# Kernel tuning notes

Hardware: AMD Instinct MI355X
Metric: run time of the kernel (lower is better)

## Reference

```python
import jax, jax.numpy as jnp
import numpy as np

D1, D2, DK, NH = 1024, 1024, 1024, 1
B, S = 4, 2048


def setup_inputs() -> dict:
    key = jax.random.key(0)
    ks = jax.random.split(key, 12)
    scale1 = 1.0 / np.sqrt(D1)
    scale2 = 1.0 / np.sqrt(D2)
    scalek = 1.0 / np.sqrt(DK)
    return {
        "x": jax.random.normal(ks[0], (B, S, D1), dtype=jnp.float32),
        "y": jax.random.normal(ks[1], (B, S, D2), dtype=jnp.float32),
        "adj": jax.random.uniform(ks[2], (B, S, S), dtype=jnp.float32),
        "Wq": jax.random.uniform(ks[3], (D1, DK), jnp.float32, -scale1, scale1),
        "bq": jax.random.uniform(ks[4], (DK,), jnp.float32, -scale1, scale1),
        "Wk": jax.random.uniform(ks[5], (D2, DK), jnp.float32, -scale2, scale2),
        "bk": jax.random.uniform(ks[6], (DK,), jnp.float32, -scale2, scale2),
        "Wv": jax.random.uniform(ks[7], (D2, DK), jnp.float32, -scale2, scale2),
        "bv": jax.random.uniform(ks[8], (DK,), jnp.float32, -scale2, scale2),
        "Wo": jax.random.uniform(ks[9], (DK, D2), jnp.float32, -scalek, scalek),
        "bo": jax.random.uniform(ks[10], (D2,), jnp.float32, -scalek, scalek),
    }


def reference(x, y, adj, Wq, bq, Wk, bk, Wv, bv, Wo, bo):
    # Single-head (n_heads=1) cross-attention with additive adjacency bias.
    dk_head = DK // NH
    norm = 1.0 / np.sqrt(DK)
    Q = (x @ Wq + bq).reshape(NH, B, S, dk_head)   # [h,b,s,d]
    K = (y @ Wk + bk).reshape(NH, B, S, dk_head)
    V = (y @ Wv + bv).reshape(NH, B, S, dk_head)
    att = jnp.einsum('hbsd,hbtd->hbst', Q, K) * norm  # [h,b,s,t]
    att = jax.nn.softmax(att + adj, axis=-1)          # adj [b,s,t] broadcasts over h
    tmp = jnp.einsum('hbst,hbtd->hbsd', att, V).reshape(B, S, -1)  # [b,s,dk]
    out = (tmp @ Wo + bo).reshape(-1, S, D2)
    return out
```

## Files before the change

### kernel.cpp

```cpp
#include <hip/hip_runtime.h>
#include <stdint.h>

typedef unsigned short u16;
using bf16x8 = __attribute__((ext_vector_type(8))) short;
using f32x4  = __attribute__((ext_vector_type(4))) float;

#define NORM 0.03125f

enum { M_PROJ = 0, M_EXP = 1, M_PV = 2, M_OUT = 3 };

__device__ __forceinline__ u16 f2bf(float f) {
  uint32_t u = __float_as_uint(f);
  return (u16)((u + 0x7FFFu + ((u >> 16) & 1u)) >> 16);
}

__device__ __forceinline__ void gload_lds16(const void* g, void* lds) {
  __builtin_amdgcn_global_load_lds(
      (const __attribute__((address_space(1))) uint32_t*)g,
      (__attribute__((address_space(3))) uint32_t*)lds, 16, 0, 0);
}

__global__ void k_cvt(const float* __restrict__ in, u16* __restrict__ out, int n4) {
  int i = blockIdx.x * blockDim.x + threadIdx.x;
  if (i >= n4) return;
  float4 v = ((const float4*)in)[i];
  uint32_t lo = f2bf(v.x) | ((uint32_t)f2bf(v.y) << 16);
  uint32_t hi = f2bf(v.z) | ((uint32_t)f2bf(v.w) << 16);
  ((uint2*)out)[i] = make_uint2(lo, hi);
}

__global__ void k_tc(const float* __restrict__ W0, const float* __restrict__ W1,
                     const float* __restrict__ W2, const float* __restrict__ W3,
                     u16* __restrict__ dst) {
  __shared__ float t[64][65];
  const float* W = blockIdx.z == 0 ? W0 : blockIdx.z == 1 ? W1 : blockIdx.z == 2 ? W2 : W3;
  u16* WT = dst + (size_t)blockIdx.z * (1024 * 1024);
  int c0 = blockIdx.x * 64, r0 = blockIdx.y * 64;
  int c = threadIdx.x & 63, q = threadIdx.x >> 6;
  for (int r = q; r < 64; r += 4) t[r][c] = W[(size_t)(r0 + r) * 1024 + c0 + c];
  __syncthreads();
  for (int r = q; r < 64; r += 4) WT[(size_t)(c0 + r) * 1024 + r0 + c] = f2bf(t[c][r]);
}

struct GArgs {
  const u16* A; const u16* B; int lda, ldb; long long bstrideB; int K;
  const float* bias; const float* adj; float* dpart; const float* dpart_r;
  void* C; int ldc;
  const u16* A1; const u16* B1; const u16* B2;
  const float* bias1; const float* bias2; void* C1; void* C2;
};

template <int MODE>
__global__ __launch_bounds__(256, 4) void gemm_occ(GArgs g) {
  __shared__ __align__(16) u16 As[128 * 64];
  __shared__ __align__(16) u16 Bs[128 * 64];

  const int tid = threadIdx.x;
  const int lane = tid & 63;
  const int wid = tid >> 6;
  const int wr = wid >> 1, wc = wid & 1;

  const int m0 = blockIdx.x * 128;
  const int n0 = blockIdx.y * 128;
  const int b = m0 >> 11;

  const u16* A = g.A; const u16* B = g.B;
  const float* bias = g.bias; void* C = g.C;
  int zmode = 0;
  if constexpr (MODE == M_PROJ) {
    int z = blockIdx.z; zmode = z;
    if (z == 1) { A = g.A1; B = g.B1; bias = g.bias1; C = g.C1; }
    else if (z == 2) { A = g.A1; B = g.B2; bias = g.bias2; C = g.C2; }
  }
  const int lda = g.lda, ldb = g.ldb, K = g.K;
  const u16* Bp = B + (size_t)b * g.bstrideB;

  f32x4 acc[4][4] = {};

  const int ric = lane >> 3;
  const int c8 = (lane & 7) * 8;

  const int fr = lane & 15;
  const int hi = lane >> 4;

  for (int kt = 0; kt < K; kt += 64) {
#pragma unroll
    for (int c = 0; c < 4; ++c) {
      int ch = wid * 4 + c;
      int row = ch * 8 + ric;
      int swc = c8 ^ ((row & 7) << 3);
      gload_lds16(A + (size_t)(m0 + row) * lda + kt + swc, (void*)&As[ch * 512]);
      gload_lds16(Bp + (size_t)(n0 + row) * ldb + kt + swc, (void*)&Bs[ch * 512]);
    }
    __syncthreads();
#pragma unroll
    for (int kk = 0; kk < 64; kk += 32) {
      bf16x8 af[4], bfr[4];
#pragma unroll
      for (int m = 0; m < 4; ++m) {
        int row = wr * 64 + m * 16 + fr;
        af[m] = *(const bf16x8*)__builtin_assume_aligned(
            &As[row * 64 + ((kk + hi * 8) ^ ((row & 7) << 3))], 16);
      }
#pragma unroll
      for (int n = 0; n < 4; ++n) {
        int row = wc * 64 + n * 16 + fr;
        bfr[n] = *(const bf16x8*)__builtin_assume_aligned(
            &Bs[row * 64 + ((kk + hi * 8) ^ ((row & 7) << 3))], 16);
      }
#pragma unroll
      for (int m = 0; m < 4; ++m)
#pragma unroll
        for (int n = 0; n < 4; ++n)
          acc[m][n] = __builtin_amdgcn_mfma_f32_16x16x32_bf16(af[m], bfr[n], acc[m][n], 0, 0, 0);
    }
    __syncthreads();
  }

  const int lr = lane >> 4;
  const int lc = lane & 15;

  if constexpr (MODE == M_PROJ) {
    if (zmode < 2) {
      u16* Cc = (u16*)C;
#pragma unroll
      for (int m = 0; m < 4; ++m)
#pragma unroll
        for (int n = 0; n < 4; ++n) {
          int gcol = n0 + wc * 64 + n * 16 + lc;
          float bv = bias[gcol];
#pragma unroll
          for (int r = 0; r < 4; ++r) {
            int grow = m0 + wr * 64 + m * 16 + lr * 4 + r;
            Cc[(size_t)grow * g.ldc + gcol] = f2bf(acc[m][n][r] + bv);
          }
        }
    } else {
      u16* Cc = (u16*)C;
#pragma unroll
      for (int m = 0; m < 4; ++m) {
        int grow0 = m0 + wr * 64 + m * 16 + lr * 4;
        int t0 = grow0 & 2047;
#pragma unroll
        for (int n = 0; n < 4; ++n) {
          int gcol = n0 + wc * 64 + n * 16 + lc;
          float bv = bias[gcol];
          ushort4 pk = make_ushort4(f2bf(acc[m][n][0] + bv), f2bf(acc[m][n][1] + bv),
                                    f2bf(acc[m][n][2] + bv), f2bf(acc[m][n][3] + bv));
          *(ushort4*)&Cc[((size_t)b * 1024 + gcol) * 2048 + t0] = pk;
        }
      }
    }
  } else if constexpr (MODE == M_EXP) {
    u16* Cc = (u16*)C;
    float esum[4][4] = {};
#pragma unroll
    for (int m = 0; m < 4; ++m)
#pragma unroll
      for (int n = 0; n < 4; ++n) {
        int gcol = n0 + wc * 64 + n * 16 + lc;
#pragma unroll
        for (int r = 0; r < 4; ++r) {
          int grow = m0 + wr * 64 + m * 16 + lr * 4 + r;
          float z = acc[m][n][r] * NORM + g.adj[(size_t)grow * 2048 + gcol];
          float e = __expf(z);
          Cc[(size_t)grow * 2048 + gcol] = f2bf(e);
          esum[m][r] += e;
        }
      }
    int pidx = blockIdx.y * 2 + wc;
#pragma unroll
    for (int m = 0; m < 4; ++m)
#pragma unroll
      for (int r = 0; r < 4; ++r) {
        float s = esum[m][r];
        s += __shfl_xor(s, 1); s += __shfl_xor(s, 2);
        s += __shfl_xor(s, 4); s += __shfl_xor(s, 8);
        if (lc == 0)
          g.dpart[(size_t)pidx * 8192 + (m0 + wr * 64 + m * 16 + lr * 4 + r)] = s;
      }
  } else if constexpr (MODE == M_PV) {
    __shared__ float dinv[128];
    if (tid < 128) {
      float s = 0.f;
#pragma unroll
      for (int t = 0; t < 32; ++t) s += g.dpart_r[(size_t)t * 8192 + m0 + tid];
      dinv[tid] = 1.0f / s;
    }
    __syncthreads();
    u16* Cc = (u16*)C;
#pragma unroll
    for (int m = 0; m < 4; ++m)
#pragma unroll
      for (int n = 0; n < 4; ++n) {
        int gcol = n0 + wc * 64 + n * 16 + lc;
#pragma unroll
        for (int r = 0; r < 4; ++r) {
          int lrow = wr * 64 + m * 16 + lr * 4 + r;
          Cc[(size_t)(m0 + lrow) * g.ldc + gcol] = f2bf(acc[m][n][r] * dinv[lrow]);
        }
      }
  } else {
    float* Cc = (float*)C;
#pragma unroll
    for (int m = 0; m < 4; ++m)
#pragma unroll
      for (int n = 0; n < 4; ++n) {
        int gcol = n0 + wc * 64 + n * 16 + lc;
        float bv = bias[gcol];
#pragma unroll
        for (int r = 0; r < 4; ++r) {
          int grow = m0 + wr * 64 + m * 16 + lr * 4 + r;
          Cc[(size_t)grow * g.ldc + gcol] = acc[m][n][r] + bv;
        }
      }
  }
}

extern "C" void kernel_launch(void* const* d_in, const int* in_sizes, int n_in,
                              void* d_out, int out_size, void* d_ws, size_t ws_size,
                              hipStream_t stream) {
  const float* x   = (const float*)d_in[0];
  const float* y   = (const float*)d_in[1];
  const float* adj = (const float*)d_in[2];
  const float* Wq  = (const float*)d_in[3];
  const float* bq  = (const float*)d_in[4];
  const float* Wk  = (const float*)d_in[5];
  const float* bk  = (const float*)d_in[6];
  const float* Wv  = (const float*)d_in[7];
  const float* bv  = (const float*)d_in[8];
  const float* Wo  = (const float*)d_in[9];
  const float* bo  = (const float*)d_in[10];
  float* out = (float*)d_out;

  char* ws = (char*)d_ws;
  if (ws_size < 143654912ULL) return;
  u16* xb = (u16*)(ws);
  u16* yb = (u16*)(ws + 16777216);
  u16* WT = (u16*)(ws + 33554432);
  u16* Qb = (u16*)(ws + 41943040);
  u16* Kb = (u16*)(ws + 58720256);
  u16* Vt = (u16*)(ws + 75497472);
  u16* E  = (u16*)(ws + 92274688);
  float* dpart = (float*)(ws + 125829120);
  u16* tmpb = (u16*)(ws + 126877696);

  u16* WqT = WT;
  u16* WkT = WT + 1048576;
  u16* WvT = WT + 2097152;
  u16* WoT = WT + 3145728;

  k_cvt<<<8192, 256, 0, stream>>>(x, xb, 2097152);
  k_cvt<<<8192, 256, 0, stream>>>(y, yb, 2097152);
  k_tc<<<dim3(16, 16, 4), 256, 0, stream>>>(Wq, Wk, Wv, Wo, WT);

  GArgs ga;
  ga.A = xb; ga.B = WqT; ga.lda = 1024; ga.ldb = 1024; ga.bstrideB = 0; ga.K = 1024;
  ga.bias = bq; ga.adj = nullptr; ga.dpart = nullptr; ga.dpart_r = nullptr;
  ga.C = Qb; ga.ldc = 1024;
  ga.A1 = yb; ga.B1 = WkT; ga.B2 = WvT; ga.bias1 = bk; ga.bias2 = bv;
  ga.C1 = Kb; ga.C2 = Vt;
  gemm_occ<M_PROJ><<<dim3(64, 8, 3), 256, 0, stream>>>(ga);

  GArgs ge = {};
  ge.A = Qb; ge.B = Kb; ge.lda = 1024; ge.ldb = 1024; ge.bstrideB = 2097152LL; ge.K = 1024;
  ge.bias = nullptr; ge.adj = adj; ge.dpart = dpart; ge.dpart_r = nullptr;
  ge.C = E; ge.ldc = 2048;
  gemm_occ<M_EXP><<<dim3(64, 16), 256, 0, stream>>>(ge);

  GArgs gp = {};
  gp.A = E; gp.B = Vt; gp.lda = 2048; gp.ldb = 2048; gp.bstrideB = 2097152LL; gp.K = 2048;
  gp.bias = nullptr; gp.adj = nullptr; gp.dpart = nullptr; gp.dpart_r = dpart;
  gp.C = tmpb; gp.ldc = 1024;
  gemm_occ<M_PV><<<dim3(64, 8), 256, 0, stream>>>(gp);

  GArgs go = {};
  go.A = tmpb; go.B = WoT; go.lda = 1024; go.ldb = 1024; go.bstrideB = 0; go.K = 1024;
  go.bias = bo; go.adj = nullptr; go.dpart = nullptr; go.dpart_r = nullptr;
  go.C = out; go.ldc = 1024;
  gemm_occ<M_OUT><<<dim3(64, 8), 256, 0, stream>>>(go);
}
```

Before: 219.0 us.

## Replace QK^T exp GEMM with 256x256-tile 8-wave pipelined kernel

Adds a dedicated kernel for the scores/exp stage, replacing the 128x128 generic GEMM path. It uses 256x256 tiles, 512 threads, a swizzled double-buffered LDS layout filled by direct global-to-LDS loads, and split-K-half staging with explicit vmcnt waits. It also raises wave priority around the MFMA blocks. The aim is more operand reuse per LDS byte and better overlap of loads with MFMA. The cost is a large LDS footprint that allows roughly one block per CU, and a grid of only 256 blocks.

```diff
diff --git a/kernel.cpp b/kernel.cpp
--- a/kernel.cpp
+++ b/kernel.cpp
@@ -50,6 +50,127 @@
   const float* bias1; const float* bias2; void* C1; void* C2;
 };
 
+__global__ __launch_bounds__(512, 2) void gemm8exp(
+    const u16* __restrict__ Qb, const u16* __restrict__ Kb,
+    const float* __restrict__ adj, float* __restrict__ dpart,
+    u16* __restrict__ E) {
+  __shared__ __align__(16) u16 sm[65536];
+
+  const int tid = threadIdx.x, lane = tid & 63, wid = tid >> 6;
+  const int wm = wid >> 2, wn = wid & 3;
+  const int m0 = blockIdx.x * 256;
+  const int n0 = blockIdx.y * 256;
+  const int b = m0 >> 11;
+  const u16* Bp = Kb + (size_t)b * 2097152;
+  const int NT = 16;
+
+  f32x4 acc[8][4] = {};
+
+  auto stage = [&](const u16* src, int r0, int kc, int dst_u16) {
+#pragma unroll
+    for (int j = 0; j < 2; ++j) {
+      int row = wid * 16 + j * 128 + (lane >> 2);
+      int cb = (lane & 3) * 16;
+      int csw = cb ^ ((row & 8) << 2);
+      gload_lds16(src + (size_t)(r0 + row) * 1024 + kc + (csw >> 1),
+                  (void*)&sm[dst_u16 + wid * 512 + j * 4096]);
+    }
+  };
+  auto stA = [&](int v, int kh) {
+    stage(Qb, m0, v * 64 + kh * 32, (v & 1) * 32768 + kh * 8192);
+  };
+  auto stB = [&](int v, int kh) {
+    stage(Bp, n0, v * 64 + kh * 32, (v & 1) * 32768 + 16384 + kh * 8192);
+  };
+
+  stA(0, 0); stB(0, 0); stA(0, 1); stB(0, 1);
+  stA(1, 0); stB(1, 0);
+  asm volatile("s_waitcnt vmcnt(8)" ::: "memory");
+  __builtin_amdgcn_s_barrier();
+
+  const int cb = (lane >> 4) * 16;
+  for (int u = 0; u < NT; ++u) {
+    const int base = (u & 1) * 32768;
+#pragma unroll
+    for (int ph = 0; ph < 4; ++ph) {
+      const int h = ph & 1, kh = ph >> 1;
+      bf16x8 af[4], bfr[4];
+#pragma unroll
+      for (int m = 0; m < 4; ++m) {
+        int row = wm * 128 + h * 64 + m * 16 + (lane & 15);
+        af[m] = *(const bf16x8*)__builtin_assume_aligned(
+            &sm[base + kh * 8192 + row * 32 + ((cb ^ ((row & 8) << 2)) >> 1)], 16);
+      }
+#pragma unroll
+      for (int n = 0; n < 4; ++n) {
+        int row = wn * 64 + n * 16 + (lane & 15);
+        bfr[n] = *(const bf16x8*)__builtin_assume_aligned(
+            &sm[base + 16384 + kh * 8192 + row * 32 + ((cb ^ ((row & 8) << 2)) >> 1)], 16);
+      }
+      if (ph == 0) {
+        if (u + 1 < NT) stA(u + 1, 1);
+      } else if (ph == 1) {
+        if (u + 1 < NT) {
+          stB(u + 1, 1);
+          asm volatile("s_waitcnt vmcnt(4)" ::: "memory");
+        } else {
+          asm volatile("s_waitcnt vmcnt(0)" ::: "memory");
+        }
+      } else if (ph == 2) {
+        if (u + 2 < NT) stA(u + 2, 0);
+      } else {
+        if (u + 2 < NT) stB(u + 2, 0);
+      }
+      __builtin_amdgcn_s_barrier();
+      __builtin_amdgcn_s_setprio(1);
+#pragma unroll
+      for (int m = 0; m < 4; ++m)
+#pragma unroll
+        for (int n = 0; n < 4; ++n)
+          acc[h * 4 + m][n] = __builtin_amdgcn_mfma_f32_16x16x32_bf16(
+              af[m], bfr[n], acc[h * 4 + m][n], 0, 0, 0);
+      __builtin_amdgcn_s_setprio(0);
+      __builtin_amdgcn_s_barrier();
+    }
+  }
+
+  const int lr = lane >> 4, lc = lane & 15;
+  float esum[8][4];
+#pragma unroll
+  for (int i = 0; i < 8; ++i)
+#pragma unroll
+    for (int r = 0; r < 4; ++r) esum[i][r] = 0.f;
+#pragma unroll
+  for (int i = 0; i < 8; ++i) {
+    int rowo = (i >> 2) * 64 + (i & 3) * 16;
+#pragma unroll
+    for (int n = 0; n < 4; ++n) {
+      int gcol = n0 + wn * 64 + n * 16 + lc;
+#pragma unroll
+      for (int r = 0; r < 4; ++r) {
+        int grow = m0 + wm * 128 + rowo + lr * 4 + r;
+        float z = acc[i][n][r] * NORM + adj[(size_t)grow * 2048 + gcol];
+        float e = __expf(z);
+        E[(size_t)grow * 2048 + gcol] = f2bf(e);
+        esum[i][r] += e;
+      }
+    }
+  }
+  int pidx = blockIdx.y * 4 + wn;
+#pragma unroll
+  for (int i = 0; i < 8; ++i) {
+    int rowo = (i >> 2) * 64 + (i & 3) * 16;
+#pragma unroll
+    for (int r = 0; r < 4; ++r) {
+      float s = esum[i][r];
+      s += __shfl_xor(s, 1); s += __shfl_xor(s, 2);
+      s += __shfl_xor(s, 4); s += __shfl_xor(s, 8);
+      if (lc == 0)
+        dpart[(size_t)pidx * 8192 + m0 + wm * 128 + rowo + lr * 4 + r] = s;
+    }
+  }
+}
+
 template <int MODE>
 __global__ __launch_bounds__(256, 4) void gemm_occ(GArgs g) {
   __shared__ __align__(16) u16 As[128 * 64];
@@ -151,34 +272,6 @@
         }
       }
     }
-  } else if constexpr (MODE == M_EXP) {
-    u16* Cc = (u16*)C;
-    float esum[4][4] = {};
-#pragma unroll
-    for (int m = 0; m < 4; ++m)
-#pragma unroll
-      for (int n = 0; n < 4; ++n) {
-        int gcol = n0 + wc * 64 + n * 16 + lc;
-#pragma unroll
-        for (int r = 0; r < 4; ++r) {
-          int grow = m0 + wr * 64 + m * 16 + lr * 4 + r;
-          float z = acc[m][n][r] * NORM + g.adj[(size_t)grow * 2048 + gcol];
-          float e = __expf(z);
-          Cc[(size_t)grow * 2048 + gcol] = f2bf(e);
-          esum[m][r] += e;
-        }
-      }
-    int pidx = blockIdx.y * 2 + wc;
-#pragma unroll
-    for (int m = 0; m < 4; ++m)
-#pragma unroll
-      for (int r = 0; r < 4; ++r) {
-        float s = esum[m][r];
-        s += __shfl_xor(s, 1); s += __shfl_xor(s, 2);
-        s += __shfl_xor(s, 4); s += __shfl_xor(s, 8);
-        if (lc == 0)
-          g.dpart[(size_t)pidx * 8192 + (m0 + wr * 64 + m * 16 + lr * 4 + r)] = s;
-      }
   } else if constexpr (MODE == M_PV) {
     __shared__ float dinv[128];
     if (tid < 128) {
@@ -262,11 +355,7 @@
   ga.C1 = Kb; ga.C2 = Vt;
   gemm_occ<M_PROJ><<<dim3(64, 8, 3), 256, 0, stream>>>(ga);
 
-  GArgs ge = {};
-  ge.A = Qb; ge.B = Kb; ge.lda = 1024; ge.ldb = 1024; ge.bstrideB = 2097152LL; ge.K = 1024;
-  ge.bias = nullptr; ge.adj = adj; ge.dpart = dpart; ge.dpart_r = nullptr;
-  ge.C = E; ge.ldc = 2048;
-  gemm_occ<M_EXP><<<dim3(64, 16), 256, 0, stream>>>(ge);
+  gemm8exp<<<dim3(32, 8), 512, 0, stream>>>(Qb, Kb, adj, dpart, E);
 
   GArgs gp = {};
   gp.A = E; gp.B = Vt; gp.lda = 2048; gp.ldb = 2048; gp.bstrideB = 2097152LL; gp.K = 2048;
```

After: 219.0 us. About the same (+0.0%).

## Fuse fp32-to-bf16 input conversion into projection GEMM and retile PV/out GEMMs

Applied to the files above, without the earlier changes.

Removes the two standalone conversion kernels for x and y. The projection GEMM now loads fp32 activations directly, converts them in registers and writes them to LDS, which saves a write and a re-read of 32 MB of bf16 intermediates. The PV and output GEMMs move to a 128x64 tile kernel, doubling the block count from 512 to 1024 so the GPU's compute units are better filled. A block-index remap intended to improve L2 locality is added to the exp GEMM and the new kernel. The trade-off is that the projection A-loads lose async global-to-LDS loads and become register round-trips.

```diff
diff --git a/kernel.cpp b/kernel.cpp
--- a/kernel.cpp
+++ b/kernel.cpp
@@ -7,7 +7,8 @@
 
 #define NORM 0.03125f
 
-enum { M_PROJ = 0, M_EXP = 1, M_PV = 2, M_OUT = 3 };
+enum { M_PROJ = 0, M_EXP = 1 };
+enum { M_PV = 0, M_OUT = 1 };
 
 __device__ __forceinline__ u16 f2bf(float f) {
   uint32_t u = __float_as_uint(f);
@@ -20,13 +21,11 @@
       (__attribute__((address_space(3))) uint32_t*)lds, 16, 0, 0);
 }
 
-__global__ void k_cvt(const float* __restrict__ in, u16* __restrict__ out, int n4) {
-  int i = blockIdx.x * blockDim.x + threadIdx.x;
-  if (i >= n4) return;
-  float4 v = ((const float4*)in)[i];
-  uint32_t lo = f2bf(v.x) | ((uint32_t)f2bf(v.y) << 16);
-  uint32_t hi = f2bf(v.z) | ((uint32_t)f2bf(v.w) << 16);
-  ((uint2*)out)[i] = make_uint2(lo, hi);
+__device__ __forceinline__ void remap1024(int& bx, int& by) {
+  int id = bx + (by << 6);
+  int nid = ((id & 7) << 7) + (id >> 3);
+  bx = nid & 63;
+  by = nid >> 6;
 }
 
 __global__ void k_tc(const float* __restrict__ W0, const float* __restrict__ W1,
@@ -46,7 +45,8 @@
   const u16* A; const u16* B; int lda, ldb; long long bstrideB; int K;
   const float* bias; const float* adj; float* dpart; const float* dpart_r;
   void* C; int ldc;
-  const u16* A1; const u16* B1; const u16* B2;
+  const float* Af0; const float* Af1;
+  const u16* B1; const u16* B2;
   const float* bias1; const float* bias2; void* C1; void* C2;
 };
 
@@ -60,17 +60,20 @@
   const int wid = tid >> 6;
   const int wr = wid >> 1, wc = wid & 1;
 
-  const int m0 = blockIdx.x * 128;
-  const int n0 = blockIdx.y * 128;
+  int bx = blockIdx.x, by = blockIdx.y;
+  if constexpr (MODE == M_EXP) remap1024(bx, by);
+  const int m0 = bx * 128;
+  const int n0 = by * 128;
   const int b = m0 >> 11;
 
-  const u16* A = g.A; const u16* B = g.B;
+  const u16* B = g.B;
   const float* bias = g.bias; void* C = g.C;
+  const float* Af = g.Af0;
   int zmode = 0;
   if constexpr (MODE == M_PROJ) {
     int z = blockIdx.z; zmode = z;
-    if (z == 1) { A = g.A1; B = g.B1; bias = g.bias1; C = g.C1; }
-    else if (z == 2) { A = g.A1; B = g.B2; bias = g.bias2; C = g.C2; }
+    if (z == 1) { Af = g.Af1; B = g.B1; bias = g.bias1; C = g.C1; }
+    else if (z == 2) { Af = g.Af1; B = g.B2; bias = g.bias2; C = g.C2; }
   }
   const int lda = g.lda, ldb = g.ldb, K = g.K;
   const u16* Bp = B + (size_t)b * g.bstrideB;
@@ -79,18 +82,41 @@
 
   const int ric = lane >> 3;
   const int c8 = (lane & 7) * 8;
-
   const int fr = lane & 15;
   const int hi = lane >> 4;
 
   for (int kt = 0; kt < K; kt += 64) {
-#pragma unroll
-    for (int c = 0; c < 4; ++c) {
-      int ch = wid * 4 + c;
-      int row = ch * 8 + ric;
-      int swc = c8 ^ ((row & 7) << 3);
-      gload_lds16(A + (size_t)(m0 + row) * lda + kt + swc, (void*)&As[ch * 512]);
-      gload_lds16(Bp + (size_t)(n0 + row) * ldb + kt + swc, (void*)&Bs[ch * 512]);
+    if constexpr (MODE == M_PROJ) {
+#pragma unroll
+      for (int c = 0; c < 4; ++c) {
+        int ch = wid * 4 + c;
+        int row = ch * 8 + ric;
+        int swc = c8 ^ ((row & 7) << 3);
+        gload_lds16(Bp + (size_t)(n0 + row) * ldb + kt + swc, (void*)&Bs[ch * 512]);
+      }
+#pragma unroll
+      for (int p = 0; p < 4; ++p) {
+        int row = p * 32 + (tid >> 3);
+        int cc = (tid & 7) * 8;
+        const float* src = &Af[(size_t)(m0 + row) * 1024 + kt + cc];
+        float4 v0 = *(const float4*)src;
+        float4 v1 = *(const float4*)(src + 4);
+        uint4 pk;
+        pk.x = f2bf(v0.x) | ((uint32_t)f2bf(v0.y) << 16);
+        pk.y = f2bf(v0.z) | ((uint32_t)f2bf(v0.w) << 16);
+        pk.z = f2bf(v1.x) | ((uint32_t)f2bf(v1.y) << 16);
+        pk.w = f2bf(v1.z) | ((uint32_t)f2bf(v1.w) << 16);
+        *(uint4*)&As[row * 64 + (cc ^ ((row & 7) << 3))] = pk;
+      }
+    } else {
+#pragma unroll
+      for (int c = 0; c < 4; ++c) {
+        int ch = wid * 4 + c;
+        int row = ch * 8 + ric;
+        int swc = c8 ^ ((row & 7) << 3);
+        gload_lds16(g.A + (size_t)(m0 + row) * lda + kt + swc, (void*)&As[ch * 512]);
+        gload_lds16(Bp + (size_t)(n0 + row) * ldb + kt + swc, (void*)&Bs[ch * 512]);
+      }
     }
     __syncthreads();
 #pragma unroll
@@ -151,7 +177,7 @@
         }
       }
     }
-  } else if constexpr (MODE == M_EXP) {
+  } else {
     u16* Cc = (u16*)C;
     float esum[4][4] = {};
 #pragma unroll
@@ -168,7 +194,7 @@
           esum[m][r] += e;
         }
       }
-    int pidx = blockIdx.y * 2 + wc;
+    int pidx = by * 2 + wc;
 #pragma unroll
     for (int m = 0; m < 4; ++m)
 #pragma unroll
@@ -179,7 +205,78 @@
         if (lc == 0)
           g.dpart[(size_t)pidx * 8192 + (m0 + wr * 64 + m * 16 + lr * 4 + r)] = s;
       }
-  } else if constexpr (MODE == M_PV) {
+  }
+}
+
+template <int MODE>
+__global__ __launch_bounds__(256, 4) void gemm64(GArgs g) {
+  __shared__ __align__(16) u16 As[128 * 64];
+  __shared__ __align__(16) u16 Bs[64 * 64];
+
+  const int tid = threadIdx.x;
+  const int lane = tid & 63;
+  const int wid = tid >> 6;
+
+  int bx = blockIdx.x, by = blockIdx.y;
+  remap1024(bx, by);
+  const int m0 = bx * 128;
+  const int n0 = by * 64;
+  const int b = m0 >> 11;
+
+  const int lda = g.lda, ldb = g.ldb, K = g.K;
+  const u16* Bp = g.B + (size_t)b * g.bstrideB;
+
+  f32x4 acc[2][4] = {};
+
+  const int ric = lane >> 3;
+  const int c8 = (lane & 7) * 8;
+  const int fr = lane & 15;
+  const int hi = lane >> 4;
+
+  for (int kt = 0; kt < K; kt += 64) {
+#pragma unroll
+    for (int c = 0; c < 4; ++c) {
+      int ch = wid * 4 + c;
+      int row = ch * 8 + ric;
+      int swc = c8 ^ ((row & 7) << 3);
+      gload_lds16(g.A + (size_t)(m0 + row) * lda + kt + swc, (void*)&As[ch * 512]);
+    }
+#pragma unroll
+    for (int c = 0; c < 2; ++c) {
+      int ch = wid * 2 + c;
+      int row = ch * 8 + ric;
+      int swc = c8 ^ ((row & 7) << 3);
+      gload_lds16(Bp + (size_t)(n0 + row) * ldb + kt + swc, (void*)&Bs[ch * 512]);
+    }
+    __syncthreads();
+#pragma unroll
+    for (int kk = 0; kk < 64; kk += 32) {
+      bf16x8 af[2], bfr[4];
+#pragma unroll
+      for (int m = 0; m < 2; ++m) {
+        int row = wid * 32 + m * 16 + fr;
+        af[m] = *(const bf16x8*)__builtin_assume_aligned(
+            &As[row * 64 + ((kk + hi * 8) ^ ((row & 7) << 3))], 16);
+      }
+#pragma unroll
+      for (int n = 0; n < 4; ++n) {
+        int row = n * 16 + fr;
+        bfr[n] = *(const bf16x8*)__builtin_assume_aligned(
+            &Bs[row * 64 + ((kk + hi * 8) ^ ((row & 7) << 3))], 16);
+      }
+#pragma unroll
+      for (int m = 0; m < 2; ++m)
+#pragma unroll
+        for (int n = 0; n < 4; ++n)
+          acc[m][n] = __builtin_amdgcn_mfma_f32_16x16x32_bf16(af[m], bfr[n], acc[m][n], 0, 0, 0);
+    }
+    __syncthreads();
+  }
+
+  const int lr = lane >> 4;
+  const int lc = lane & 15;
+
+  if constexpr (MODE == M_PV) {
     __shared__ float dinv[128];
     if (tid < 128) {
       float s = 0.f;
@@ -188,29 +285,29 @@
       dinv[tid] = 1.0f / s;
     }
     __syncthreads();
-    u16* Cc = (u16*)C;
-#pragma unroll
-    for (int m = 0; m < 4; ++m)
-#pragma unroll
-      for (int n = 0; n < 4; ++n) {
-        int gcol = n0 + wc * 64 + n * 16 + lc;
+    u16* Cc = (u16*)g.C;
+#pragma unroll
+    for (int m = 0; m < 2; ++m)
+#pragma unroll
+      for (int n = 0; n < 4; ++n) {
+        int gcol = n0 + n * 16 + lc;
 #pragma unroll
         for (int r = 0; r < 4; ++r) {
-          int lrow = wr * 64 + m * 16 + lr * 4 + r;
+          int lrow = wid * 32 + m * 16 + lr * 4 + r;
           Cc[(size_t)(m0 + lrow) * g.ldc + gcol] = f2bf(acc[m][n][r] * dinv[lrow]);
         }
       }
   } else {
-    float* Cc = (float*)C;
-#pragma unroll
-    for (int m = 0; m < 4; ++m)
-#pragma unroll
-      for (int n = 0; n < 4; ++n) {
-        int gcol = n0 + wc * 64 + n * 16 + lc;
-        float bv = bias[gcol];
+    float* Cc = (float*)g.C;
+#pragma unroll
+    for (int m = 0; m < 2; ++m)
+#pragma unroll
+      for (int n = 0; n < 4; ++n) {
+        int gcol = n0 + n * 16 + lc;
+        float bv = g.bias[gcol];
 #pragma unroll
         for (int r = 0; r < 4; ++r) {
-          int grow = m0 + wr * 64 + m * 16 + lr * 4 + r;
+          int grow = m0 + wid * 32 + m * 16 + lr * 4 + r;
           Cc[(size_t)grow * g.ldc + gcol] = acc[m][n][r] + bv;
         }
       }
@@ -235,8 +332,6 @@
 
   char* ws = (char*)d_ws;
   if (ws_size < 143654912ULL) return;
-  u16* xb = (u16*)(ws);
-  u16* yb = (u16*)(ws + 16777216);
   u16* WT = (u16*)(ws + 33554432);
   u16* Qb = (u16*)(ws + 41943040);
   u16* Kb = (u16*)(ws + 58720256);
@@ -250,33 +345,28 @@
   u16* WvT = WT + 2097152;
   u16* WoT = WT + 3145728;
 
-  k_cvt<<<8192, 256, 0, stream>>>(x, xb, 2097152);
-  k_cvt<<<8192, 256, 0, stream>>>(y, yb, 2097152);
   k_tc<<<dim3(16, 16, 4), 256, 0, stream>>>(Wq, Wk, Wv, Wo, WT);
 
-  GArgs ga;
-  ga.A = xb; ga.B = WqT; ga.lda = 1024; ga.ldb = 1024; ga.bstrideB = 0; ga.K = 1024;
-  ga.bias = bq; ga.adj = nullptr; ga.dpart = nullptr; ga.dpart_r = nullptr;
-  ga.C = Qb; ga.ldc = 1024;
-  ga.A1 = yb; ga.B1 = WkT; ga.B2 = WvT; ga.bias1 = bk; ga.bias2 = bv;
+  GArgs ga = {};
+  ga.lda = 1024; ga.ldb = 1024; ga.bstrideB = 0; ga.K = 1024;
+  ga.B = WqT; ga.bias = bq; ga.C = Qb; ga.ldc = 1024;
+  ga.Af0 = x; ga.Af1 = y;
+  ga.B1 = WkT; ga.B2 = WvT; ga.bias1 = bk; ga.bias2 = bv;
   ga.C1 = Kb; ga.C2 = Vt;
   gemm_occ<M_PROJ><<<dim3(64, 8, 3), 256, 0, stream>>>(ga);
 
   GArgs ge = {};
   ge.A = Qb; ge.B = Kb; ge.lda = 1024; ge.ldb = 1024; ge.bstrideB = 2097152LL; ge.K = 1024;
-  ge.bias = nullptr; ge.adj = adj; ge.dpart = dpart; ge.dpart_r = nullptr;
-  ge.C = E; ge.ldc = 2048;
+  ge.adj = adj; ge.dpart = dpart; ge.C = E; ge.ldc = 2048;
   gemm_occ<M_EXP><<<dim3(64, 16), 256, 0, stream>>>(ge);
 
   GArgs gp = {};
   gp.A = E; gp.B = Vt; gp.lda = 2048; gp.ldb = 2048; gp.bstrideB = 2097152LL; gp.K = 2048;
-  gp.bias = nullptr; gp.adj = nullptr; gp.dpart = nullptr; gp.dpart_r = dpart;
-  gp.C = tmpb; gp.ldc = 1024;
-  gemm_occ<M_PV><<<dim3(64, 8), 256, 0, stream>>>(gp);
+  gp.dpart_r = dpart; gp.C = tmpb; gp.ldc = 1024;
+  gemm64<M_PV><<<dim3(64, 16), 256, 0, stream>>>(gp);
 
   GArgs go = {};
   go.A = tmpb; go.B = WoT; go.lda = 1024; go.ldb = 1024; go.bstrideB = 0; go.K = 1024;
-  go.bias = bo; go.adj = nullptr; go.dpart = nullptr; go.dpart_r = nullptr;
-  go.C = out; go.ldc = 1024;
-  gemm_occ<M_OUT><<<dim3(64, 8), 256, 0, stream>>>(go);
-}
+  go.bias = bo; go.C = out; go.ldc = 1024;
+  gemm64<M_OUT><<<dim3(64, 16), 256, 0, stream>>>(go);
+}
```

New measurement: 327.7 us. +49.6%, slower.
